# Performance work log

Measured on AMD Instinct MI355X. Metric: run time of the kernel, lower is better.

## Reference

```python
import jax, jax.numpy as jnp
import numpy as np

DIM = 64
NUM_HEAD = 8
SIZES = [3, 5, 7]
GROUPS = [2, 1, 1]
G_DIM = DIM // 4
SPLITS = [G_DIM * n for n in GROUPS]  # [32, 16, 16]


def _dwconv(x, w, k):
    # depthwise conv, NCHW, kernel (C,1,k,k), groups=C, same padding
    return jax.lax.conv_general_dilated(
        x, w, window_strides=(1, 1), padding=[(k // 2, k // 2)] * 2,
        dimension_numbers=('NCHW', 'OIHW', 'NCHW'),
        feature_group_count=x.shape[1])


def _conv1x1(x, w):
    # w: (out, in)
    return jnp.einsum('oi,bihw->bohw', w, x)


def _avgpool2(x):
    b, c, h, w = x.shape
    return x.reshape(b, c, h // 2, 2, w // 2, 2).mean(axis=(3, 5))


def _l2norm(x, eps=1e-12):
    n = jnp.sqrt(jnp.sum(x * x, axis=-1, keepdims=True))
    return x / jnp.maximum(n, eps)


def setup_inputs() -> dict:
    key = jax.random.key(0)
    ks = jax.random.split(key, 20)
    s = 0.05
    inp = {
        'x': jax.random.normal(ks[0], (4, DIM, 256, 256), dtype=jnp.float32),
        'y': jax.random.normal(ks[1], (4, DIM, 256, 256), dtype=jnp.float32),
    }
    i = 2
    for pfx in ('hp1', 'hp2'):
        for kk, ch in zip(SIZES, SPLITS):
            inp[f'{pfx}_w{kk}'] = jax.random.normal(ks[i], (ch, 1, kk, kk), dtype=jnp.float32) * s
            i += 1
    for name in ('qh_w', 'kh_w', 'vh_w', 'ql_w', 'kl_w', 'vl_w', 'proj_w'):
        inp[name] = jax.random.normal(ks[i], (DIM, DIM), dtype=jnp.float32) * s
        i += 1
    inp['attn_w1'] = jax.random.normal(ks[i], (DIM // 4, DIM), dtype=jnp.float32) * s; i += 1
    inp['attn_w2'] = jax.random.normal(ks[i], (DIM, DIM // 4), dtype=jnp.float32) * s; i += 1
    inp['temperature'] = jnp.ones((NUM_HEAD, 1, 1), dtype=jnp.float32)
    return inp


def reference(x, y, hp1_w3, hp1_w5, hp1_w7, hp2_w3, hp2_w5, hp2_w7,
              qh_w, kh_w, vh_w, ql_w, kl_w, vl_w, proj_w,
              attn_w1, attn_w2, temperature):
    b, c, h, w = x.shape
    idx = np.cumsum(SPLITS)[:-1].tolist()
    xs = jnp.split(x, idx, axis=1)
    ys = jnp.split(y, idx, axis=1)
    hp1 = [hp1_w3, hp1_w5, hp1_w7]
    hp2 = [hp2_w3, hp2_w5, hp2_w7]
    x_h = jnp.concatenate([_dwconv(xs[i], hp1[i], SIZES[i]) for i in range(3)], axis=1)
    y_h = jnp.concatenate([_dwconv(ys[i], hp2[i], SIZES[i]) for i in range(3)], axis=1)
    q_h = _conv1x1(x_h, qh_w)
    k_h = _conv1x1(y_h, kh_w)
    v_h = _conv1x1(x_h, vh_w)
    pooled = jnp.mean(q_h * k_h, axis=(2, 3), keepdims=True)  # b,c,1,1
    high_att = jnp.tanh(_conv1x1(jax.nn.relu(_conv1x1(pooled, attn_w1)), attn_w2))
    out_h = high_att * v_h
    q_l = _conv1x1(_avgpool2(x), ql_w)
    k_l = _conv1x1(_avgpool2(y), kl_w)
    v_l = _conv1x1(y, vl_w)
    ch = c // NUM_HEAD
    q_l = q_l.reshape(b, NUM_HEAD, ch, -1)  # b head c (h/2*w/2)
    k_l = k_l.reshape(b, NUM_HEAD, ch, -1)
    v_l = v_l.reshape(b, NUM_HEAD, ch, -1)  # b head c (h*w)
    q_l = _l2norm(q_l)
    k_l = _l2norm(k_l)
    low_att = jnp.einsum('bhcn,bhdn->bhcd', q_l, k_l) * temperature
    low_att = jax.nn.softmax(low_att, axis=-1)
    out_l = jnp.einsum('bhcd,bhdn->bhcn', low_att, v_l).reshape(b, c, h, w)
    return _conv1x1(out_h + out_l, proj_w)
```

## Files before the change

kernel.cpp:

```cpp
#include <hip/hip_runtime.h>
#include <hip/hip_bf16.h>
#include <math.h>

#define NPX   65536
#define IMGST 4194304
#define NB    4

template<int K, int RT>
__device__ __forceinline__ void dw_strip(const float* __restrict__ in,
                                         const float* __restrict__ wp,
                                         float* __restrict__ outp,
                                         int rowS, int c4) {
    float w[K * K];
#pragma unroll
    for (int i = 0; i < K * K; ++i) w[i] = wp[i];

    float acc[RT][4];
#pragma unroll
    for (int i = 0; i < RT; ++i)
#pragma unroll
        for (int j = 0; j < 4; ++j) acc[i][j] = 0.f;

    const bool lok = (c4 != 0);
    const bool rok = (c4 < 252);
    const int off0 = lok ? -4 : 0;
    const int off2 = rok ? 4 : 0;

#pragma unroll
    for (int ri = 0; ri < RT + K - 1; ++ri) {
        const int gr = rowS - K / 2 + ri;
        float v[12];
        if ((unsigned)gr < 256u) {
            const float* rp = in + gr * 256 + c4;
            const float4 m0 = *reinterpret_cast<const float4*>(rp + off0);
            const float4 m1 = *reinterpret_cast<const float4*>(rp);
            const float4 m2 = *reinterpret_cast<const float4*>(rp + off2);
            v[0] = lok ? m0.x : 0.f; v[1] = lok ? m0.y : 0.f;
            v[2] = lok ? m0.z : 0.f; v[3] = lok ? m0.w : 0.f;
            v[4] = m1.x; v[5] = m1.y; v[6] = m1.z; v[7] = m1.w;
            v[8] = rok ? m2.x : 0.f;  v[9] = rok ? m2.y : 0.f;
            v[10] = rok ? m2.z : 0.f; v[11] = rok ? m2.w : 0.f;
        } else {
#pragma unroll
            for (int t = 0; t < 12; ++t) v[t] = 0.f;
        }
#pragma unroll
        for (int i = 0; i < RT; ++i) {
            const int dy = ri - i;
            if (dy >= 0 && dy < K) {
#pragma unroll
                for (int dx = 0; dx < K; ++dx) {
                    const float wv = w[dy * K + dx];
#pragma unroll
                    for (int j = 0; j < 4; ++j)
                        acc[i][j] = fmaf(wv, v[j + dx + 4 - K / 2], acc[i][j]);
                }
            }
        }
    }

    float* obase = outp + (size_t)rowS * 256 + c4;
#pragma unroll
    for (int i = 0; i < RT; ++i) {
        float4 o;
        o.x = acc[i][0]; o.y = acc[i][1]; o.z = acc[i][2]; o.w = acc[i][3];
        *reinterpret_cast<float4*>(obase + i * 256) = o;
    }
}

__global__ __launch_bounds__(256) void dsattn_dwconv2(
        const float* __restrict__ xin, const float* __restrict__ yin,
        float* __restrict__ xout, float* __restrict__ yout,
        const float* __restrict__ x3, const float* __restrict__ x5,
        const float* __restrict__ x7, const float* __restrict__ y3,
        const float* __restrict__ y5, const float* __restrict__ y7) {
    const int tid = threadIdx.x;
    const int xcd = blockIdx.x & 7;
    const int v   = blockIdx.x >> 3;
    const int sel = blockIdx.y >> 2;
    const int b   = blockIdx.y & 3;
    const int tc = tid & 63, tr = tid >> 6;
    const int c4 = tc * 4;

    const float* inb = (sel == 0 ? xin : yin) + (size_t)b * IMGST;
    float* outb      = (sel == 0 ? xout : yout) + (size_t)b * IMGST;

    if (v < 64) {
        const int idx = xcd * 64 + v;
        const int c = 48 + (idx >> 5), band = idx & 31;
        const float* w = (sel == 0 ? x7 : y7) + (c - 48) * 49;
        dw_strip<7, 2>(inb + (size_t)c * NPX, w, outb + (size_t)c * NPX,
                       band * 8 + tr * 2, c4);
    } else if (v < 128) {
        const int idx = xcd * 64 + (v - 64);
        const int c = idx >> 4, band = idx & 15;
        const float* w = (sel == 0 ? x3 : y3) + c * 9;
        dw_strip<3, 4>(inb + (size_t)c * NPX, w, outb + (size_t)c * NPX,
                       band * 16 + tr * 4, c4);
    } else {
        const int idx = xcd * 32 + (v - 128);
        const int c = 32 + (idx >> 4), band = idx & 15;
        const float* w = (sel == 0 ? x5 : y5) + (c - 32) * 25;
        dw_strip<5, 4>(inb + (size_t)c * NPX, w, outb + (size_t)c * NPX,
                       band * 16 + tr * 4, c4);
    }
}

__global__ __launch_bounds__(256) void dsattn_crossgram(
        const float* __restrict__ xh, const float* __restrict__ yh,
        float* __restrict__ Spart) {
    __shared__ float sx[64 * 65];
    __shared__ float sy[64 * 65];
    const int tid = threadIdx.x;
    const int chunk = blockIdx.x;
    const int b = blockIdx.y;
    const int rt = tid >> 4;
    const int ct = tid & 15;
    float acc[16];
#pragma unroll
    for (int i = 0; i < 16; ++i) acc[i] = 0.f;
    const size_t ibase = (size_t)b * IMGST + chunk * 512;

    for (int tile = 0; tile < 8; ++tile) {
        __syncthreads();
        for (int idx = tid; idx < 1024; idx += 256) {
            const int c = idx >> 4, p4 = (idx & 15) * 4;
            const size_t g = ibase + (size_t)c * NPX + tile * 64 + p4;
            const float4 vx = *reinterpret_cast<const float4*>(&xh[g]);
            const float4 vy = *reinterpret_cast<const float4*>(&yh[g]);
            sx[(p4 + 0) * 65 + c] = vx.x; sx[(p4 + 1) * 65 + c] = vx.y;
            sx[(p4 + 2) * 65 + c] = vx.z; sx[(p4 + 3) * 65 + c] = vx.w;
            sy[(p4 + 0) * 65 + c] = vy.x; sy[(p4 + 1) * 65 + c] = vy.y;
            sy[(p4 + 2) * 65 + c] = vy.z; sy[(p4 + 3) * 65 + c] = vy.w;
        }
        __syncthreads();
        for (int p = 0; p < 64; ++p) {
            float xr[4], yc[4];
#pragma unroll
            for (int j = 0; j < 4; ++j) {
                xr[j] = sx[p * 65 + rt * 4 + j];
                yc[j] = sy[p * 65 + ct * 4 + j];
            }
#pragma unroll
            for (int r = 0; r < 4; ++r)
#pragma unroll
                for (int c2 = 0; c2 < 4; ++c2)
                    acc[r * 4 + c2] = fmaf(xr[r], yc[c2], acc[r * 4 + c2]);
        }
    }
    float* outp = Spart + ((size_t)b * 128 + chunk) * 4096;
#pragma unroll
    for (int r = 0; r < 4; ++r)
#pragma unroll
        for (int c2 = 0; c2 < 4; ++c2)
            outp[(rt * 4 + r) * 64 + ct * 4 + c2] = acc[r * 4 + c2];
}

__global__ __launch_bounds__(256) void dsattn_reduceS(
        const float* __restrict__ Spart, float* __restrict__ Sred) {
    const int i = blockIdx.x * 256 + threadIdx.x;
    const int b = blockIdx.y;
    const float* p = Spart + (size_t)b * 128 * 4096 + i;
    float s = 0.f;
#pragma unroll 4
    for (int k = 0; k < 128; ++k) s += p[(size_t)k * 4096];
    Sred[b * 4096 + i] = s;
}

__global__ __launch_bounds__(256) void dsattn_poolgram(
        const float* __restrict__ x, const float* __restrict__ y,
        float* __restrict__ Ppart) {
    __shared__ float sx[64 * 65];
    __shared__ float sy[64 * 65];
    const int tid = threadIdx.x;
    const int irow = blockIdx.x;
    const int b = blockIdx.y;
    const int rt = tid >> 4, ct = tid & 15;
    float aXY[16], aXX[16], aYY[16];
#pragma unroll
    for (int i = 0; i < 16; ++i) { aXY[i] = 0.f; aXX[i] = 0.f; aYY[i] = 0.f; }
    const size_t ibase = (size_t)b * IMGST + (size_t)(2 * irow) * 256;

    for (int tile = 0; tile < 2; ++tile) {
        __syncthreads();
        for (int idx = tid; idx < 4096; idx += 256) {
            const int c = idx >> 6, jj = idx & 63;
            const size_t g = ibase + (size_t)c * NPX + 2 * (tile * 64 + jj);
            const float2 a0 = *reinterpret_cast<const float2*>(x + g);
            const float2 a1 = *reinterpret_cast<const float2*>(x + g + 256);
            const float2 b0 = *reinterpret_cast<const float2*>(y + g);
            const float2 b1 = *reinterpret_cast<const float2*>(y + g + 256);
            sx[jj * 65 + c] = 0.25f * (a0.x + a0.y + a1.x + a1.y);
            sy[jj * 65 + c] = 0.25f * (b0.x + b0.y + b1.x + b1.y);
        }
        __syncthreads();
        for (int p = 0; p < 64; ++p) {
            float xr[4], xc[4], yr[4], yc[4];
#pragma unroll
            for (int j = 0; j < 4; ++j) {
                xr[j] = sx[p * 65 + rt * 4 + j];
                xc[j] = sx[p * 65 + ct * 4 + j];
                yr[j] = sy[p * 65 + rt * 4 + j];
                yc[j] = sy[p * 65 + ct * 4 + j];
            }
#pragma unroll
            for (int r = 0; r < 4; ++r)
#pragma unroll
                for (int c2 = 0; c2 < 4; ++c2) {
                    aXY[r * 4 + c2] = fmaf(xr[r], yc[c2], aXY[r * 4 + c2]);
                    aXX[r * 4 + c2] = fmaf(xr[r], xc[c2], aXX[r * 4 + c2]);
                    aYY[r * 4 + c2] = fmaf(yr[r], yc[c2], aYY[r * 4 + c2]);
                }
        }
    }
    float* outp = Ppart + ((size_t)b * 128 + irow) * 12288;
#pragma unroll
    for (int r = 0; r < 4; ++r)
#pragma unroll
        for (int c2 = 0; c2 < 4; ++c2) {
            const int o = (rt * 4 + r) * 64 + ct * 4 + c2;
            outp[o]        = aXY[r * 4 + c2];
            outp[4096 + o] = aXX[r * 4 + c2];
            outp[8192 + o] = aYY[r * 4 + c2];
        }
}

__global__ __launch_bounds__(256) void dsattn_reduceP(
        const float* __restrict__ Ppart, float* __restrict__ Pred) {
    const int i = blockIdx.x * 256 + threadIdx.x;
    const int b = blockIdx.y;
    const float* p = Ppart + (size_t)b * 128 * 12288 + i;
    float s = 0.f;
#pragma unroll 4
    for (int k = 0; k < 128; ++k) s += p[(size_t)k * 12288];
    Pred[b * 12288 + i] = s;
}

__global__ __launch_bounds__(256) void dsattn_sandwich(
        const float* __restrict__ Pred, const float* __restrict__ Sred,
        const float* __restrict__ wql, const float* __restrict__ wkl,
        const float* __restrict__ wq,  const float* __restrict__ wk,
        float* __restrict__ nq2g, float* __restrict__ nk2g,
        float* __restrict__ Gg, float* __restrict__ pooledg) {
    __shared__ float Wl[64 * 65];
    __shared__ float Sl[64 * 65];
    __shared__ float Tl[64 * 65];
    __shared__ float red[256];
    const int unit = blockIdx.x, b = blockIdx.y, tid = threadIdx.x;
    const float *W1, *W2, *Sg;
    if (unit == 0)      { W1 = wql; W2 = wql; Sg = Pred + (size_t)b * 12288 + 4096; }
    else if (unit == 1) { W1 = wkl; W2 = wkl; Sg = Pred + (size_t)b * 12288 + 8192; }
    else if (unit == 2) { W1 = wql; W2 = wkl; Sg = Pred + (size_t)b * 12288; }
    else                { W1 = wq;  W2 = wk;  Sg = Sred + (size_t)b * 4096; }

    for (int i = tid; i < 4096; i += 256) {
        const int r = i >> 6, c = i & 63;
        Wl[r * 65 + c] = W1[i];
        Sl[r * 65 + c] = Sg[i];
    }
    __syncthreads();

    const int rt = tid >> 4, ct = tid & 15;
    float acc[16];
#pragma unroll
    for (int i = 0; i < 16; ++i) acc[i] = 0.f;
    for (int cc = 0; cc < 64; ++cc) {
        float wr[4], sc[4];
#pragma unroll
        for (int j = 0; j < 4; ++j) {
            wr[j] = Wl[(rt * 4 + j) * 65 + cc];
            sc[j] = Sl[cc * 65 + ct * 4 + j];
        }
#pragma unroll
        for (int r = 0; r < 4; ++r)
#pragma unroll
            for (int c2 = 0; c2 < 4; ++c2)
                acc[r * 4 + c2] = fmaf(wr[r], sc[c2], acc[r * 4 + c2]);
    }
#pragma unroll
    for (int r = 0; r < 4; ++r)
#pragma unroll
        for (int c2 = 0; c2 < 4; ++c2)
            Tl[(rt * 4 + r) * 65 + ct * 4 + c2] = acc[r * 4 + c2];
    __syncthreads();
    for (int i = tid; i < 4096; i += 256) Sl[(i >> 6) * 65 + (i & 63)] = W2[i];
    __syncthreads();

    if (unit == 2) {
        for (int i = tid; i < 512; i += 256) {
            const int h = i >> 6, r = (i >> 3) & 7, d = i & 7;
            float s = 0.f;
#pragma unroll
            for (int c = 0; c < 64; ++c)
                s = fmaf(Tl[(h * 8 + r) * 65 + c], Sl[(h * 8 + d) * 65 + c], s);
            Gg[b * 512 + i] = s;
        }
    } else {
        const int r = tid >> 2, part = tid & 3;
        float s = 0.f;
#pragma unroll
        for (int q = 0; q < 16; ++q) {
            const int cp = part * 16 + q;
            s = fmaf(Tl[r * 65 + cp], Sl[r * 65 + cp], s);
        }
        red[tid] = s;
        __syncthreads();
        if (tid < 64) {
            const float v = red[tid * 4] + red[tid * 4 + 1] + red[tid * 4 + 2] + red[tid * 4 + 3];
            if (unit == 0)      nq2g[b * 64 + tid] = v;
            else if (unit == 1) nk2g[b * 64 + tid] = v;
            else                pooledg[b * 64 + tid] = v * (1.f / 65536.f);
        }
    }
}

__global__ __launch_bounds__(256) void dsattn_smallmid(
        const float* __restrict__ nq2g, const float* __restrict__ nk2g,
        const float* __restrict__ Gg, const float* __restrict__ pooledg,
        const float* __restrict__ temp, const float* __restrict__ w1,
        const float* __restrict__ w2, const float* __restrict__ wvl,
        float* __restrict__ hattg, float* __restrict__ tvlg) {
    __shared__ float att[512];
    __shared__ float z[16];
    const int b = blockIdx.x, tid = threadIdx.x;
    if (tid < 16) {
        float a = 0.f;
#pragma unroll
        for (int c = 0; c < 64; ++c) a = fmaf(w1[tid * 64 + c], pooledg[b * 64 + c], a);
        z[tid] = fmaxf(a, 0.f);
    }
    if (tid < 64) {
        const int h = tid >> 3;
        const float tpr = temp[h];
        const float nq = fmaxf(sqrtf(nq2g[b * 64 + tid]), 1e-12f);
        float a[8], m = -1e30f;
#pragma unroll
        for (int d = 0; d < 8; ++d) {
            const float nk = fmaxf(sqrtf(nk2g[b * 64 + h * 8 + d]), 1e-12f);
            a[d] = Gg[b * 512 + tid * 8 + d] / (nq * nk) * tpr;
            m = fmaxf(m, a[d]);
        }
        float ssum = 0.f;
#pragma unroll
        for (int d = 0; d < 8; ++d) { a[d] = expf(a[d] - m); ssum += a[d]; }
        const float inv = 1.f / ssum;
#pragma unroll
        for (int d = 0; d < 8; ++d) att[tid * 8 + d] = a[d] * inv;
    }
    __syncthreads();
    if (tid < 64) {
        float a = 0.f;
#pragma unroll
        for (int i = 0; i < 16; ++i) a = fmaf(w2[tid * 16 + i], z[i], a);
        hattg[b * 64 + tid] = tanhf(a);
    }
    for (int i = tid; i < 4096; i += 256) {
        const int m = i >> 6, c = i & 63, h = m >> 3;
        float s = 0.f;
#pragma unroll
        for (int d = 0; d < 8; ++d) s = fmaf(att[m * 8 + d], wvl[(h * 8 + d) * 64 + c], s);
        tvlg[b * 4096 + i] = s;
    }
}

__global__ __launch_bounds__(256) void dsattn_fold(
        const float* __restrict__ wproj, const float* __restrict__ wvh,
        const float* __restrict__ hattg, const float* __restrict__ tvlg,
        float* __restrict__ At, float* __restrict__ Bt) {
    __shared__ float Pl[64 * 65];
    __shared__ float Vl[64 * 65];
    __shared__ float hm[64];
    const int unit = blockIdx.x, b = blockIdx.y, tid = threadIdx.x;
    if (tid < 64) hm[tid] = hattg[b * 64 + tid];
    for (int i = tid; i < 4096; i += 256) Pl[(i >> 6) * 65 + (i & 63)] = wproj[i];
    __syncthreads();
    for (int i = tid; i < 4096; i += 256) {
        const int m = i >> 6, c = i & 63;
        Vl[m * 65 + c] = (unit == 0) ? hm[m] * wvh[i] : tvlg[b * 4096 + i];
    }
    __syncthreads();

    const int rt = tid >> 4, ct = tid & 15;
    float acc[16];
#pragma unroll
    for (int i = 0; i < 16; ++i) acc[i] = 0.f;
    for (int m = 0; m < 64; ++m) {
        float pv[4], vv[4];
#pragma unroll
        for (int j = 0; j < 4; ++j) {
            pv[j] = Pl[(ct * 4 + j) * 65 + m];
            vv[j] = Vl[m * 65 + rt * 4 + j];
        }
#pragma unroll
        for (int r = 0; r < 4; ++r)
#pragma unroll
            for (int c2 = 0; c2 < 4; ++c2)
                acc[r * 4 + c2] = fmaf(pv[c2], vv[r], acc[r * 4 + c2]);
    }
    float* outp = ((unit == 0) ? At : Bt) + (size_t)b * 4096;
#pragma unroll
    for (int r = 0; r < 4; ++r)
#pragma unroll
        for (int c2 = 0; c2 < 4; ++c2)
            outp[(rt * 4 + r) * 64 + ct * 4 + c2] = acc[r * 4 + c2];
}

__global__ __launch_bounds__(256, 4) void dsattn_final(
        const float* __restrict__ xh, const float* __restrict__ y,
        const float* __restrict__ At, const float* __restrict__ Bt,
        float* __restrict__ out) {
    const int tid = threadIdx.x;
    const int b = blockIdx.y;
    const int lane = tid & 63;
    const int oc0 = __builtin_amdgcn_readfirstlane((tid >> 6) * 16);
    const size_t base = (size_t)b * IMGST + (size_t)blockIdx.x * 256 + lane * 4;
    const float* __restrict__ Ab = At + b * 4096 + oc0;
    const float* __restrict__ Bb = Bt + b * 4096 + oc0;

    float acc[16][4];
#pragma unroll
    for (int j = 0; j < 16; ++j)
#pragma unroll
        for (int k = 0; k < 4; ++k) acc[j][k] = 0.f;

#pragma unroll 2
    for (int c = 0; c < 64; ++c) {
        const float4 xv = *reinterpret_cast<const float4*>(xh + base + (size_t)c * NPX);
        const float4 yv = *reinterpret_cast<const float4*>(y  + base + (size_t)c * NPX);
#pragma unroll
        for (int j = 0; j < 16; ++j) {
            const float a  = Ab[c * 64 + j];
            const float bb = Bb[c * 64 + j];
            acc[j][0] = fmaf(a, xv.x, acc[j][0]);
            acc[j][1] = fmaf(a, xv.y, acc[j][1]);
            acc[j][2] = fmaf(a, xv.z, acc[j][2]);
            acc[j][3] = fmaf(a, xv.w, acc[j][3]);
            acc[j][0] = fmaf(bb, yv.x, acc[j][0]);
            acc[j][1] = fmaf(bb, yv.y, acc[j][1]);
            acc[j][2] = fmaf(bb, yv.z, acc[j][2]);
            acc[j][3] = fmaf(bb, yv.w, acc[j][3]);
        }
    }

    float* op = out + base;
#pragma unroll
    for (int j = 0; j < 16; ++j) {
        float4 v;
        v.x = acc[j][0]; v.y = acc[j][1]; v.z = acc[j][2]; v.w = acc[j][3];
        *reinterpret_cast<float4*>(op + (size_t)(oc0 + j) * NPX) = v;
    }
}

extern "C" void kernel_launch(void* const* d_in, const int* in_sizes, int n_in,
                              void* d_out, int out_size, void* d_ws, size_t ws_size,
                              hipStream_t stream) {
    const float* x      = (const float*)d_in[0];
    const float* y      = (const float*)d_in[1];
    const float* hp1_w3 = (const float*)d_in[2];
    const float* hp1_w5 = (const float*)d_in[3];
    const float* hp1_w7 = (const float*)d_in[4];
    const float* hp2_w3 = (const float*)d_in[5];
    const float* hp2_w5 = (const float*)d_in[6];
    const float* hp2_w7 = (const float*)d_in[7];
    const float* qh_w   = (const float*)d_in[8];
    const float* kh_w   = (const float*)d_in[9];
    const float* vh_w   = (const float*)d_in[10];
    const float* ql_w   = (const float*)d_in[11];
    const float* kl_w   = (const float*)d_in[12];
    const float* vl_w   = (const float*)d_in[13];
    const float* proj_w = (const float*)d_in[14];
    const float* attn_w1 = (const float*)d_in[15];
    const float* attn_w2 = (const float*)d_in[16];
    const float* temperature = (const float*)d_in[17];

    float* out = (float*)d_out;

    float* xh     = (float*)d_ws;
    float* Spart  = xh + (size_t)NB * IMGST;
    float* small  = Spart + (size_t)4 * 128 * 4096;
    float* Sred   = small;
    float* Pred   = Sred + 16384;
    float* nq2    = Pred + 49152;
    float* nk2    = nq2 + 256;
    float* G      = nk2 + 256;
    float* pooled = G + 2048;
    float* hatt   = pooled + 256;
    float* tvl    = hatt + 256;
    float* At     = tvl + 16384;
    float* Bt     = At + 16384;

    float* yh    = out;
    float* Ppart = out;

    dsattn_dwconv2<<<dim3(1280, 8), 256, 0, stream>>>(x, y, xh, yh,
                                                      hp1_w3, hp1_w5, hp1_w7,
                                                      hp2_w3, hp2_w5, hp2_w7);
    dsattn_crossgram<<<dim3(128, 4), 256, 0, stream>>>(xh, yh, Spart);
    dsattn_reduceS<<<dim3(16, 4), 256, 0, stream>>>(Spart, Sred);
    dsattn_poolgram<<<dim3(128, 4), 256, 0, stream>>>(x, y, Ppart);
    dsattn_reduceP<<<dim3(48, 4), 256, 0, stream>>>(Ppart, Pred);
    dsattn_sandwich<<<dim3(4, 4), 256, 0, stream>>>(Pred, Sred, ql_w, kl_w, qh_w, kh_w,
                                                    nq2, nk2, G, pooled);
    dsattn_smallmid<<<4, 256, 0, stream>>>(nq2, nk2, G, pooled, temperature,
                                           attn_w1, attn_w2, vl_w, hatt, tvl);
    dsattn_fold<<<dim3(2, 4), 256, 0, stream>>>(proj_w, vh_w, hatt, tvl, At, Bt);
    dsattn_final<<<dim3(256, 4), 256, 0, stream>>>(xh, y, At, Bt, out);
}
```

Measured before the change: 259.8 us.

## Fuse 2x2 average pooling into depthwise conv pass and feed pooled gram

The depthwise conv kernel now also computes 2x2 average-pooled x and y from the rows it already loads and writes them to a workspace buffer. The pooled-gram kernel then reads these quarter-size pooled tensors instead of re-reading the full x and y inputs, which cuts that stage's global memory traffic. The fused path runs only when the workspace is large enough; otherwise it falls back to the original kernel. In exchange, the conv pass carries extra registers and writes extra data.

```diff
diff --git a/kernel.cpp b/kernel.cpp
--- a/kernel.cpp
+++ b/kernel.cpp
@@ -5,12 +5,15 @@
 #define NPX   65536
 #define IMGST 4194304
 #define NB    4
+#define PPLANE 16384
+#define PIMG   1048576
 
 template<int K, int RT>
 __device__ __forceinline__ void dw_strip(const float* __restrict__ in,
                                          const float* __restrict__ wp,
                                          float* __restrict__ outp,
-                                         int rowS, int c4) {
+                                         int rowS, int c4,
+                                         float* __restrict__ pb, int do_pool) {
     float w[K * K];
 #pragma unroll
     for (int i = 0; i < K * K; ++i) w[i] = wp[i];
@@ -20,6 +23,10 @@
     for (int i = 0; i < RT; ++i)
 #pragma unroll
         for (int j = 0; j < 4; ++j) acc[i][j] = 0.f;
+
+    float pool[RT / 2][2];
+#pragma unroll
+    for (int i = 0; i < RT / 2; ++i) { pool[i][0] = 0.f; pool[i][1] = 0.f; }
 
     const bool lok = (c4 != 0);
     const bool rok = (c4 < 252);
@@ -44,6 +51,13 @@
 #pragma unroll
             for (int t = 0; t < 12; ++t) v[t] = 0.f;
         }
+        {
+            const int ib = ri - K / 2;
+            if (ib >= 0 && ib < RT) {
+                pool[ib >> 1][0] += v[4] + v[5];
+                pool[ib >> 1][1] += v[6] + v[7];
+            }
+        }
 #pragma unroll
         for (int i = 0; i < RT; ++i) {
             const int dy = ri - i;
@@ -65,6 +79,16 @@
         float4 o;
         o.x = acc[i][0]; o.y = acc[i][1]; o.z = acc[i][2]; o.w = acc[i][3];
         *reinterpret_cast<float4*>(obase + i * 256) = o;
+    }
+    if (do_pool) {
+        const int pr0 = rowS >> 1, pc = c4 >> 1;
+#pragma unroll
+        for (int i = 0; i < RT / 2; ++i) {
+            float2 p;
+            p.x = 0.25f * pool[i][0];
+            p.y = 0.25f * pool[i][1];
+            *reinterpret_cast<float2*>(pb + (size_t)(pr0 + i) * 128 + pc) = p;
+        }
     }
 }
 
@@ -73,7 +97,8 @@
         float* __restrict__ xout, float* __restrict__ yout,
         const float* __restrict__ x3, const float* __restrict__ x5,
         const float* __restrict__ x7, const float* __restrict__ y3,
-        const float* __restrict__ y5, const float* __restrict__ y7) {
+        const float* __restrict__ y5, const float* __restrict__ y7,
+        float* __restrict__ xbar, float* __restrict__ ybar, int do_pool) {
     const int tid = threadIdx.x;
     const int xcd = blockIdx.x & 7;
     const int v   = blockIdx.x >> 3;
@@ -84,25 +109,26 @@
 
     const float* inb = (sel == 0 ? xin : yin) + (size_t)b * IMGST;
     float* outb      = (sel == 0 ? xout : yout) + (size_t)b * IMGST;
+    float* pbb       = (sel == 0 ? xbar : ybar) + (size_t)b * PIMG;
 
     if (v < 64) {
         const int idx = xcd * 64 + v;
         const int c = 48 + (idx >> 5), band = idx & 31;
         const float* w = (sel == 0 ? x7 : y7) + (c - 48) * 49;
         dw_strip<7, 2>(inb + (size_t)c * NPX, w, outb + (size_t)c * NPX,
-                       band * 8 + tr * 2, c4);
+                       band * 8 + tr * 2, c4, pbb + (size_t)c * PPLANE, do_pool);
     } else if (v < 128) {
         const int idx = xcd * 64 + (v - 64);
         const int c = idx >> 4, band = idx & 15;
         const float* w = (sel == 0 ? x3 : y3) + c * 9;
         dw_strip<3, 4>(inb + (size_t)c * NPX, w, outb + (size_t)c * NPX,
-                       band * 16 + tr * 4, c4);
+                       band * 16 + tr * 4, c4, pbb + (size_t)c * PPLANE, do_pool);
     } else {
         const int idx = xcd * 32 + (v - 128);
         const int c = 32 + (idx >> 4), band = idx & 15;
         const float* w = (sel == 0 ? x5 : y5) + (c - 32) * 25;
         dw_strip<5, 4>(inb + (size_t)c * NPX, w, outb + (size_t)c * NPX,
-                       band * 16 + tr * 4, c4);
+                       band * 16 + tr * 4, c4, pbb + (size_t)c * PPLANE, do_pool);
     }
 }
 
@@ -167,7 +193,61 @@
     Sred[b * 4096 + i] = s;
 }
 
-__global__ __launch_bounds__(256) void dsattn_poolgram(
+__global__ __launch_bounds__(256) void dsattn_poolgram_pp(
+        const float* __restrict__ xbar, const float* __restrict__ ybar,
+        float* __restrict__ Ppart) {
+    __shared__ float sx[64 * 65];
+    __shared__ float sy[64 * 65];
+    const int tid = threadIdx.x;
+    const int irow = blockIdx.x;
+    const int b = blockIdx.y;
+    const int rt = tid >> 4, ct = tid & 15;
+    float aXY[16], aXX[16], aYY[16];
+#pragma unroll
+    for (int i = 0; i < 16; ++i) { aXY[i] = 0.f; aXX[i] = 0.f; aYY[i] = 0.f; }
+    const size_t pbase = (size_t)b * PIMG + (size_t)irow * 128;
+
+    for (int tile = 0; tile < 2; ++tile) {
+        __syncthreads();
+        for (int idx = tid; idx < 4096; idx += 256) {
+            const int c = idx >> 6, jj = idx & 63;
+            const size_t g = pbase + (size_t)c * PPLANE + tile * 64 + jj;
+            sx[jj * 65 + c] = xbar[g];
+            sy[jj * 65 + c] = ybar[g];
+        }
+        __syncthreads();
+        for (int p = 0; p < 64; ++p) {
+            float xr[4], xc[4], yr[4], yc[4];
+#pragma unroll
+            for (int j = 0; j < 4; ++j) {
+                xr[j] = sx[p * 65 + rt * 4 + j];
+                xc[j] = sx[p * 65 + ct * 4 + j];
+                yr[j] = sy[p * 65 + rt * 4 + j];
+                yc[j] = sy[p * 65 + ct * 4 + j];
+            }
+#pragma unroll
+            for (int r = 0; r < 4; ++r)
+#pragma unroll
+                for (int c2 = 0; c2 < 4; ++c2) {
+                    aXY[r * 4 + c2] = fmaf(xr[r], yc[c2], aXY[r * 4 + c2]);
+                    aXX[r * 4 + c2] = fmaf(xr[r], xc[c2], aXX[r * 4 + c2]);
+                    aYY[r * 4 + c2] = fmaf(yr[r], yc[c2], aYY[r * 4 + c2]);
+                }
+        }
+    }
+    float* outp = Ppart + ((size_t)b * 128 + irow) * 12288;
+#pragma unroll
+    for (int r = 0; r < 4; ++r)
+#pragma unroll
+        for (int c2 = 0; c2 < 4; ++c2) {
+            const int o = (rt * 4 + r) * 64 + ct * 4 + c2;
+            outp[o]        = aXY[r * 4 + c2];
+            outp[4096 + o] = aXX[r * 4 + c2];
+            outp[8192 + o] = aYY[r * 4 + c2];
+        }
+}
+
+__global__ __launch_bounds__(256) void dsattn_poolgram_xy(
         const float* __restrict__ x, const float* __restrict__ y,
         float* __restrict__ Ppart) {
     __shared__ float sx[64 * 65];
@@ -477,8 +557,7 @@
 
     float* xh     = (float*)d_ws;
     float* Spart  = xh + (size_t)NB * IMGST;
-    float* small  = Spart + (size_t)4 * 128 * 4096;
-    float* Sred   = small;
+    float* Sred   = Spart + (size_t)4 * 128 * 4096;
     float* Pred   = Sred + 16384;
     float* nq2    = Pred + 49152;
     float* nk2    = nq2 + 256;
@@ -488,16 +567,26 @@
     float* tvl    = hatt + 256;
     float* At     = tvl + 16384;
     float* Bt     = At + 16384;
+    float* wsend  = Bt + 16384;
+    float* xbar   = wsend;
+    float* ybar   = xbar + (size_t)NB * PIMG;
+
+    const size_t need_fused = (size_t)(18992128 + 2 * NB * PIMG) * sizeof(float);
+    const int fused = (ws_size >= need_fused) ? 1 : 0;
 
     float* yh    = out;
     float* Ppart = out;
 
     dsattn_dwconv2<<<dim3(1280, 8), 256, 0, stream>>>(x, y, xh, yh,
                                                       hp1_w3, hp1_w5, hp1_w7,
-                                                      hp2_w3, hp2_w5, hp2_w7);
+                                                      hp2_w3, hp2_w5, hp2_w7,
+                                                      xbar, ybar, fused);
     dsattn_crossgram<<<dim3(128, 4), 256, 0, stream>>>(xh, yh, Spart);
     dsattn_reduceS<<<dim3(16, 4), 256, 0, stream>>>(Spart, Sred);
-    dsattn_poolgram<<<dim3(128, 4), 256, 0, stream>>>(x, y, Ppart);
+    if (fused)
+        dsattn_poolgram_pp<<<dim3(128, 4), 256, 0, stream>>>(xbar, ybar, Ppart);
+    else
+        dsattn_poolgram_xy<<<dim3(128, 4), 256, 0, stream>>>(x, y, Ppart);
     dsattn_reduceP<<<dim3(48, 4), 256, 0, stream>>>(Ppart, Pred);
     dsattn_sandwich<<<dim3(4, 4), 256, 0, stream>>>(Pred, Sred, ql_w, kl_w, qh_w, kh_w,
                                                     nq2, nk2, G, pooled);
```

Result: slower. 266.5 us (+2.6%).

## Fuse pooled-gram into depthwise conv launch and merge the two reductions

Applied to the files above, without the earlier changes.

Folds the pooled Gram computation into the depthwise-conv kernel as 64 extra block columns (512 blocks), so both passes over x and y share one launch and can overlap. The two partial-sum reduction kernels are merged into one launch. Ppart moves from the output buffer into a separate workspace region, because yh now occupies the output while the pooled blocks run. This removes two launches and their gaps, but adds shared memory to the conv kernel's footprint, which may lower occupancy for the conv blocks.

```diff
diff --git a/kernel.cpp b/kernel.cpp
--- a/kernel.cpp
+++ b/kernel.cpp
@@ -68,15 +68,80 @@
     }
 }
 
-__global__ __launch_bounds__(256) void dsattn_dwconv2(
+__device__ __forceinline__ void poolgram_body(
+        const float* __restrict__ x, const float* __restrict__ y,
+        float* __restrict__ Ppart, int irow, int b, int tid) {
+    __shared__ float sx[64 * 65];
+    __shared__ float sy[64 * 65];
+    const int rt = tid >> 4, ct = tid & 15;
+    float aXY[16], aXX[16], aYY[16];
+#pragma unroll
+    for (int i = 0; i < 16; ++i) { aXY[i] = 0.f; aXX[i] = 0.f; aYY[i] = 0.f; }
+    const size_t ibase = (size_t)b * IMGST + (size_t)(2 * irow) * 256;
+
+    for (int tile = 0; tile < 2; ++tile) {
+        __syncthreads();
+        for (int idx = tid; idx < 4096; idx += 256) {
+            const int c = idx >> 6, jj = idx & 63;
+            const size_t g = ibase + (size_t)c * NPX + 2 * (tile * 64 + jj);
+            const float2 a0 = *reinterpret_cast<const float2*>(x + g);
+            const float2 a1 = *reinterpret_cast<const float2*>(x + g + 256);
+            const float2 b0 = *reinterpret_cast<const float2*>(y + g);
+            const float2 b1 = *reinterpret_cast<const float2*>(y + g + 256);
+            sx[jj * 65 + c] = 0.25f * (a0.x + a0.y + a1.x + a1.y);
+            sy[jj * 65 + c] = 0.25f * (b0.x + b0.y + b1.x + b1.y);
+        }
+        __syncthreads();
+        for (int p = 0; p < 64; ++p) {
+            float xr[4], xc[4], yr[4], yc[4];
+#pragma unroll
+            for (int j = 0; j < 4; ++j) {
+                xr[j] = sx[p * 65 + rt * 4 + j];
+                xc[j] = sx[p * 65 + ct * 4 + j];
+                yr[j] = sy[p * 65 + rt * 4 + j];
+                yc[j] = sy[p * 65 + ct * 4 + j];
+            }
+#pragma unroll
+            for (int r = 0; r < 4; ++r)
+#pragma unroll
+                for (int c2 = 0; c2 < 4; ++c2) {
+                    aXY[r * 4 + c2] = fmaf(xr[r], yc[c2], aXY[r * 4 + c2]);
+                    aXX[r * 4 + c2] = fmaf(xr[r], xc[c2], aXX[r * 4 + c2]);
+                    aYY[r * 4 + c2] = fmaf(yr[r], yc[c2], aYY[r * 4 + c2]);
+                }
+        }
+    }
+    float* outp = Ppart + ((size_t)b * 128 + irow) * 12288;
+#pragma unroll
+    for (int r = 0; r < 4; ++r)
+#pragma unroll
+        for (int c2 = 0; c2 < 4; ++c2) {
+            const int o = (rt * 4 + r) * 64 + ct * 4 + c2;
+            outp[o]        = aXY[r * 4 + c2];
+            outp[4096 + o] = aXX[r * 4 + c2];
+            outp[8192 + o] = aYY[r * 4 + c2];
+        }
+}
+
+__global__ __launch_bounds__(256) void dsattn_dwpool(
         const float* __restrict__ xin, const float* __restrict__ yin,
         float* __restrict__ xout, float* __restrict__ yout,
         const float* __restrict__ x3, const float* __restrict__ x5,
         const float* __restrict__ x7, const float* __restrict__ y3,
-        const float* __restrict__ y5, const float* __restrict__ y7) {
+        const float* __restrict__ y5, const float* __restrict__ y7,
+        float* __restrict__ Ppart) {
     const int tid = threadIdx.x;
-    const int xcd = blockIdx.x & 7;
-    const int v   = blockIdx.x >> 3;
+    const int xb = blockIdx.x;
+
+    if (xb >= 1280) {
+        const int irow = (xb - 1280) * 2 + (blockIdx.y >> 2);
+        const int b = blockIdx.y & 3;
+        poolgram_body(xin, yin, Ppart, irow, b, tid);
+        return;
+    }
+
+    const int xcd = xb & 7;
+    const int v   = xb >> 3;
     const int sel = blockIdx.y >> 2;
     const int b   = blockIdx.y & 3;
     const int tc = tid & 63, tr = tid >> 6;
@@ -156,84 +221,25 @@
             outp[(rt * 4 + r) * 64 + ct * 4 + c2] = acc[r * 4 + c2];
 }
 
-__global__ __launch_bounds__(256) void dsattn_reduceS(
-        const float* __restrict__ Spart, float* __restrict__ Sred) {
-    const int i = blockIdx.x * 256 + threadIdx.x;
+__global__ __launch_bounds__(256) void dsattn_reduceSP(
+        const float* __restrict__ Spart, float* __restrict__ Sred,
+        const float* __restrict__ Ppart, float* __restrict__ Pred) {
     const int b = blockIdx.y;
-    const float* p = Spart + (size_t)b * 128 * 4096 + i;
-    float s = 0.f;
+    if (blockIdx.x < 16) {
+        const int i = blockIdx.x * 256 + threadIdx.x;
+        const float* p = Spart + (size_t)b * 128 * 4096 + i;
+        float s = 0.f;
 #pragma unroll 4
-    for (int k = 0; k < 128; ++k) s += p[(size_t)k * 4096];
-    Sred[b * 4096 + i] = s;
-}
-
-__global__ __launch_bounds__(256) void dsattn_poolgram(
-        const float* __restrict__ x, const float* __restrict__ y,
-        float* __restrict__ Ppart) {
-    __shared__ float sx[64 * 65];
-    __shared__ float sy[64 * 65];
-    const int tid = threadIdx.x;
-    const int irow = blockIdx.x;
-    const int b = blockIdx.y;
-    const int rt = tid >> 4, ct = tid & 15;
-    float aXY[16], aXX[16], aYY[16];
-#pragma unroll
-    for (int i = 0; i < 16; ++i) { aXY[i] = 0.f; aXX[i] = 0.f; aYY[i] = 0.f; }
-    const size_t ibase = (size_t)b * IMGST + (size_t)(2 * irow) * 256;
-
-    for (int tile = 0; tile < 2; ++tile) {
-        __syncthreads();
-        for (int idx = tid; idx < 4096; idx += 256) {
-            const int c = idx >> 6, jj = idx & 63;
-            const size_t g = ibase + (size_t)c * NPX + 2 * (tile * 64 + jj);
-            const float2 a0 = *reinterpret_cast<const float2*>(x + g);
-            const float2 a1 = *reinterpret_cast<const float2*>(x + g + 256);
-            const float2 b0 = *reinterpret_cast<const float2*>(y + g);
-            const float2 b1 = *reinterpret_cast<const float2*>(y + g + 256);
-            sx[jj * 65 + c] = 0.25f * (a0.x + a0.y + a1.x + a1.y);
-            sy[jj * 65 + c] = 0.25f * (b0.x + b0.y + b1.x + b1.y);
-        }
-        __syncthreads();
-        for (int p = 0; p < 64; ++p) {
-            float xr[4], xc[4], yr[4], yc[4];
-#pragma unroll
-            for (int j = 0; j < 4; ++j) {
-                xr[j] = sx[p * 65 + rt * 4 + j];
-                xc[j] = sx[p * 65 + ct * 4 + j];
-                yr[j] = sy[p * 65 + rt * 4 + j];
-                yc[j] = sy[p * 65 + ct * 4 + j];
-            }
-#pragma unroll
-            for (int r = 0; r < 4; ++r)
-#pragma unroll
-                for (int c2 = 0; c2 < 4; ++c2) {
-                    aXY[r * 4 + c2] = fmaf(xr[r], yc[c2], aXY[r * 4 + c2]);
-                    aXX[r * 4 + c2] = fmaf(xr[r], xc[c2], aXX[r * 4 + c2]);
-                    aYY[r * 4 + c2] = fmaf(yr[r], yc[c2], aYY[r * 4 + c2]);
-                }
-        }
-    }
-    float* outp = Ppart + ((size_t)b * 128 + irow) * 12288;
-#pragma unroll
-    for (int r = 0; r < 4; ++r)
-#pragma unroll
-        for (int c2 = 0; c2 < 4; ++c2) {
-            const int o = (rt * 4 + r) * 64 + ct * 4 + c2;
-            outp[o]        = aXY[r * 4 + c2];
-            outp[4096 + o] = aXX[r * 4 + c2];
-            outp[8192 + o] = aYY[r * 4 + c2];
-        }
-}
-
-__global__ __launch_bounds__(256) void dsattn_reduceP(
-        const float* __restrict__ Ppart, float* __restrict__ Pred) {
-    const int i = blockIdx.x * 256 + threadIdx.x;
-    const int b = blockIdx.y;
-    const float* p = Ppart + (size_t)b * 128 * 12288 + i;
-    float s = 0.f;
+        for (int k = 0; k < 128; ++k) s += p[(size_t)k * 4096];
+        Sred[b * 4096 + i] = s;
+    } else {
+        const int i = (blockIdx.x - 16) * 256 + threadIdx.x;
+        const float* p = Ppart + (size_t)b * 128 * 12288 + i;
+        float s = 0.f;
 #pragma unroll 4
-    for (int k = 0; k < 128; ++k) s += p[(size_t)k * 12288];
-    Pred[b * 12288 + i] = s;
+        for (int k = 0; k < 128; ++k) s += p[(size_t)k * 12288];
+        Pred[b * 12288 + i] = s;
+    }
 }
 
 __global__ __launch_bounds__(256) void dsattn_sandwich(
@@ -477,8 +483,7 @@
 
     float* xh     = (float*)d_ws;
     float* Spart  = xh + (size_t)NB * IMGST;
-    float* small  = Spart + (size_t)4 * 128 * 4096;
-    float* Sred   = small;
+    float* Sred   = Spart + (size_t)4 * 128 * 4096;
     float* Pred   = Sred + 16384;
     float* nq2    = Pred + 49152;
     float* nk2    = nq2 + 256;
@@ -488,17 +493,16 @@
     float* tvl    = hatt + 256;
     float* At     = tvl + 16384;
     float* Bt     = At + 16384;
-
-    float* yh    = out;
-    float* Ppart = out;
-
-    dsattn_dwconv2<<<dim3(1280, 8), 256, 0, stream>>>(x, y, xh, yh,
-                                                      hp1_w3, hp1_w5, hp1_w7,
-                                                      hp2_w3, hp2_w5, hp2_w7);
+    float* Ppart  = Bt + 16384;
+
+    float* yh = out;
+
+    dsattn_dwpool<<<dim3(1344, 8), 256, 0, stream>>>(x, y, xh, yh,
+                                                     hp1_w3, hp1_w5, hp1_w7,
+                                                     hp2_w3, hp2_w5, hp2_w7,
+                                                     Ppart);
     dsattn_crossgram<<<dim3(128, 4), 256, 0, stream>>>(xh, yh, Spart);
-    dsattn_reduceS<<<dim3(16, 4), 256, 0, stream>>>(Spart, Sred);
-    dsattn_poolgram<<<dim3(128, 4), 256, 0, stream>>>(x, y, Ppart);
-    dsattn_reduceP<<<dim3(48, 4), 256, 0, stream>>>(Ppart, Pred);
+    dsattn_reduceSP<<<dim3(64, 4), 256, 0, stream>>>(Spart, Sred, Ppart, Pred);
     dsattn_sandwich<<<dim3(4, 4), 256, 0, stream>>>(Pred, Sred, ql_w, kl_w, qh_w, kh_w,
                                                     nq2, nk2, G, pooled);
     dsattn_smallmid<<<4, 256, 0, stream>>>(nq2, nk2, G, pooled, temperature,
```

Result: slower. 266.7 us (+2.6%).
